# Performance work log

Measured on AMD Instinct MI355X. Metric: run time of the kernel, lower is better.

## Reference

```python
import jax, jax.numpy as jnp
import numpy as np

HIDDEN = 1024
HEADS = 16
HEAD = HIDDEN // HEADS


def setup_inputs() -> dict:
    key = jax.random.key(0)
    k1, k2, k3, k4, k5, k6 = jax.random.split(key, 6)
    B, S = 2, 2048
    x = jax.random.normal(k1, (B, S, HIDDEN), dtype=jnp.float32)
    mask = jax.random.randint(k2, (B, S), 0, 2, dtype=jnp.int32)
    # torch nn.Linear params: W [out,in], b [out]
    s = 1.0 / np.sqrt(HIDDEN)
    qkv_w = jax.random.uniform(k3, (3 * HIDDEN, HIDDEN), jnp.float32, -s, s)
    qkv_b = jax.random.uniform(k4, (3 * HIDDEN,), jnp.float32, -s, s)
    out_w = jax.random.uniform(k5, (HIDDEN, HIDDEN), jnp.float32, -s, s)
    out_b = jax.random.uniform(k6, (HIDDEN,), jnp.float32, -s, s)
    return {"x": x, "mask": mask, "qkv_w": qkv_w, "qkv_b": qkv_b,
            "out_w": out_w, "out_b": out_b}


def reference(x, mask, qkv_w, qkv_b, out_w, out_b):
    B, S, H = x.shape
    scale = HEAD ** -0.5
    qkv = x @ qkv_w.T + qkv_b                      # [B,S,3H]
    qkv = qkv.reshape(B, S, 3, HEADS, HEAD)
    qkv = jnp.transpose(qkv, (2, 0, 3, 1, 4))      # [3,B,h,S,d]
    q, k, v = qkv[0], qkv[1], qkv[2]
    scores = jnp.einsum('bhqd,bhkd->bhqk', q, k) * scale
    # key-padding mask [B,S] -> [B,1,1,S]
    scores = jnp.where(mask[:, None, None, :] == 0, -1e9, scores)
    attn = jax.nn.softmax(scores, axis=-1)
    # dropout is identity in eval mode
    ctx = jnp.einsum('bhqk,bhkd->bhqd', attn, v)   # [B,h,S,d]
    ctx = jnp.transpose(ctx, (0, 2, 1, 3)).reshape(B, S, H)
    return ctx @ out_w.T + out_b
```

## Files before the change

### kernel.cpp

```cpp
#include <hip/hip_runtime.h>
#include <hip/hip_bf16.h>

#define S_LEN 2048
#define NH    16
#define HD    64
#define HID   1024
#define BATCH 2
#define STK   72

typedef __bf16 bf16x8 __attribute__((ext_vector_type(8)));
typedef float  f32x4  __attribute__((ext_vector_type(4)));

__device__ __forceinline__ unsigned int pk2(float lo, float hi) {
    union { __hip_bfloat162 h; unsigned int u; } c;
    c.h = __float22bfloat162_rn(make_float2(lo, hi));
    return c.u;
}
__device__ __forceinline__ uint4 pk8(float4 a, float4 b) {
    uint4 o;
    o.x = pk2(a.x, a.y); o.y = pk2(a.z, a.w);
    o.z = pk2(b.x, b.y); o.w = pk2(b.z, b.w);
    return o;
}
__device__ __forceinline__ float exp2_hw(float x) {
    float r; asm("v_exp_f32 %0, %1" : "=v"(r) : "v"(x)); return r;
}
__device__ __forceinline__ void gll16(const unsigned short* g, unsigned short* l) {
    __builtin_amdgcn_global_load_lds(
        (const __attribute__((address_space(1))) void*)g,
        (__attribute__((address_space(3))) void*)l, 16, 0, 0);
}

__global__ __launch_bounds__(256)
void fill_constf(float* __restrict__ out, long n, float v) {
    long i = (long)blockIdx.x * 256 + threadIdx.x;
    const long stride = (long)gridDim.x * 256;
    for (; i < n; i += stride) out[i] = v;
}

__global__ __launch_bounds__(256)
void cvt_bf16(const float* __restrict__ src, unsigned short* __restrict__ dst, long n8) {
    long t = (long)blockIdx.x * 256 + threadIdx.x;
    const long stride = (long)gridDim.x * 256;
    for (; t < n8; t += stride) {
        const float4 a = *(const float4*)(src + t * 8);
        const float4 b = *(const float4*)(src + t * 8 + 4);
        *(uint4*)(dst + t * 8) = pk8(a, b);
    }
}
__global__ __launch_bounds__(256)
void cvt2_bf16(const float* __restrict__ s0, unsigned short* __restrict__ d0, long n0,
               const float* __restrict__ s1, unsigned short* __restrict__ d1, long n1) {
    long t = (long)blockIdx.x * 256 + threadIdx.x;
    const long stride = (long)gridDim.x * 256;
    for (; t < n0 + n1; t += stride) {
        const float* s; unsigned short* d; long i;
        if (t < n0) { s = s0; d = d0; i = t; } else { s = s1; d = d1; i = t - n0; }
        const float4 a = *(const float4*)(s + i * 8);
        const float4 b = *(const float4*)(s + i * 8 + 4);
        *(uint4*)(d + i * 8) = pk8(a, b);
    }
}

__global__ __launch_bounds__(256)
void gemm_bf16(const unsigned short* __restrict__ A,
               const unsigned short* __restrict__ W,
               const float* __restrict__ bias,
               unsigned short* __restrict__ o0,
               unsigned short* __restrict__ o1,
               unsigned short* __restrict__ o2,
               float* __restrict__ of,
               int mode)
{
    __shared__ __align__(16) unsigned short lA[128 * 32];
    __shared__ __align__(16) unsigned short lB[128 * 32];
    const int tid  = threadIdx.x;
    const int lane = tid & 63, wv = tid >> 6;
    const int quad = lane >> 4, l16 = lane & 15;
    const int wm = (wv & 1) * 64, wn = (wv >> 1) * 64;
    const int m0 = blockIdx.y * 128, n0 = blockIdx.x * 128;

    f32x4 acc[4][4] = {};

    const int srow0 = wv * 32 + (lane >> 2);
    const int srow1 = srow0 + 16;
    const int sc    = (lane & 3) * 8;
    const unsigned short* pa0 = A + (long)(m0 + srow0) * HID + sc;
    const unsigned short* pa1 = A + (long)(m0 + srow1) * HID + sc;
    const unsigned short* pb0 = W + (long)(n0 + srow0) * HID + sc;
    const unsigned short* pb1 = W + (long)(n0 + srow1) * HID + sc;
    unsigned short* la0 = &lA[(wv * 2 + 0) * 512];
    unsigned short* la1 = &lA[(wv * 2 + 1) * 512];
    unsigned short* lb0 = &lB[(wv * 2 + 0) * 512];
    unsigned short* lb1 = &lB[(wv * 2 + 1) * 512];

    for (int k0 = 0; k0 < HID; k0 += 32) {
        gll16(pa0 + k0, la0);
        gll16(pa1 + k0, la1);
        gll16(pb0 + k0, lb0);
        gll16(pb1 + k0, lb1);
        __syncthreads();

        bf16x8 af[4], bfr[4];
#pragma unroll
        for (int mt = 0; mt < 4; mt++)
            af[mt] = *(const bf16x8*)&lA[(wm + mt * 16 + l16) * 32 + quad * 8];
#pragma unroll
        for (int nt = 0; nt < 4; nt++)
            bfr[nt] = *(const bf16x8*)&lB[(wn + nt * 16 + l16) * 32 + quad * 8];
#pragma unroll
        for (int mt = 0; mt < 4; mt++)
#pragma unroll
            for (int nt = 0; nt < 4; nt++)
                acc[mt][nt] = __builtin_amdgcn_mfma_f32_16x16x32_bf16(
                    af[mt], bfr[nt], acc[mt][nt], 0, 0, 0);
        __syncthreads();
    }

    if (mode == 0) {
#pragma unroll
        for (int nt = 0; nt < 4; nt++) {
            const int n = n0 + wn + nt * 16 + l16;
            const float bv = bias[n];
            const int part = n >> 10, f = n & 1023, h = f >> 6, d = f & 63;
#pragma unroll
            for (int mt = 0; mt < 4; mt++) {
                const int mbase = m0 + wm + mt * 16 + quad * 4;
                const int b = mbase >> 11, s0 = mbase & 2047;
                const int bh = b * NH + h;
                if (part == 2) {
                    uint2 o;
                    o.x = pk2(acc[mt][nt][0] + bv, acc[mt][nt][1] + bv);
                    o.y = pk2(acc[mt][nt][2] + bv, acc[mt][nt][3] + bv);
                    *(uint2*)&o2[((long)bh * HD + d) * S_LEN + s0] = o;
                } else {
                    unsigned short* dst = (part == 0) ? o0 : o1;
#pragma unroll
                    for (int r = 0; r < 4; r++) {
                        union { __hip_bfloat16 h; unsigned short u; } cv;
                        cv.h = __float2bfloat16(acc[mt][nt][r] + bv);
                        dst[((long)bh * S_LEN + s0 + r) * HD + d] = cv.u;
                    }
                }
            }
        }
    } else {
#pragma unroll
        for (int nt = 0; nt < 4; nt++) {
            const int n = n0 + wn + nt * 16 + l16;
            const float bv = bias[n];
#pragma unroll
            for (int mt = 0; mt < 4; mt++) {
                const int mbase = m0 + wm + mt * 16 + quad * 4;
#pragma unroll
                for (int r = 0; r < 4; r++)
                    of[(long)(mbase + r) * HID + n] = acc[mt][nt][r] + bv;
            }
        }
    }
}

__global__ __launch_bounds__(512)
void attn(const unsigned short* __restrict__ q,
          const unsigned short* __restrict__ k,
          const unsigned short* __restrict__ vt_g,
          const int* __restrict__ mask,
          unsigned short* __restrict__ ctx)
{
    __shared__ __align__(16) unsigned short kt[64 * STK];
    __shared__ __align__(16) unsigned short vt[64 * STK];
    __shared__ __align__(16) __bf16 pt[8][16 * 72];
    __shared__ float mkv[64];

    const int tid  = threadIdx.x;
    const int lane = tid & 63, wv = tid >> 6;
    const int quad = lane >> 4, l16 = lane & 15;
    const int qt = blockIdx.x, h = blockIdx.y, b = blockIdx.z;
    const int bh = b * NH + h;
    const float SC = 0.18033688f;

    const int sq = qt * 128 + wv * 16 + l16;
    bf16x8 qf0 = *(const bf16x8*)&q[((long)bh * S_LEN + sq) * HD + quad * 8];
    bf16x8 qf1 = *(const bf16x8*)&q[((long)bh * S_LEN + sq) * HD + 32 + quad * 8];

    float mrun = -1e30f, lrun = 0.f;
    f32x4 Of[4] = {};

    const int sr = tid >> 3, sc8 = (tid & 7) * 8;
    const unsigned short* kg = k    + ((long)bh * S_LEN + sr) * HD + sc8;
    const unsigned short* vg = vt_g + ((long)bh * HD + sr) * S_LEN + sc8;
    __bf16* ptw = pt[wv];

    uint4 rk = *(const uint4*)(kg);
    uint4 rv = *(const uint4*)(vg);
    float rm = 0.f;
    if (tid < 64) rm = (mask[b * S_LEN + tid] == 0) ? -1e9f : 0.f;

    for (int k0 = 0; k0 < S_LEN; k0 += 64) {
        *(uint4*)&kt[sr * STK + sc8] = rk;
        *(uint4*)&vt[sr * STK + sc8] = rv;
        if (tid < 64) mkv[tid] = rm;
        if (k0 + 64 < S_LEN) {
            rk = *(const uint4*)(kg + (long)(k0 + 64) * HD);
            rv = *(const uint4*)(vg + (k0 + 64));
            if (tid < 64) rm = (mask[b * S_LEN + k0 + 64 + tid] == 0) ? -1e9f : 0.f;
        }
        __syncthreads();

        float st[4][4];
#pragma unroll
        for (int nt = 0; nt < 4; nt++) {
            bf16x8 k0f = *(const bf16x8*)&kt[(nt * 16 + l16) * STK + quad * 8];
            bf16x8 k1f = *(const bf16x8*)&kt[(nt * 16 + l16) * STK + 32 + quad * 8];
            f32x4 s = {};
            s = __builtin_amdgcn_mfma_f32_16x16x32_bf16(k0f, qf0, s, 0, 0, 0);
            s = __builtin_amdgcn_mfma_f32_16x16x32_bf16(k1f, qf1, s, 0, 0, 0);
            const float4 mv = *(const float4*)&mkv[nt * 16 + quad * 4];
#pragma unroll
            for (int r = 0; r < 4; r++) st[nt][r] = fmaf(s[r], SC, (&mv.x)[r]);
        }

        float mx = st[0][0];
#pragma unroll
        for (int nt = 0; nt < 4; nt++)
#pragma unroll
            for (int r = 0; r < 4; r++) mx = fmaxf(mx, st[nt][r]);
        mx = fmaxf(mx, __shfl_xor(mx, 16, 64));
        mx = fmaxf(mx, __shfl_xor(mx, 32, 64));
        const float mn = fmaxf(mrun, mx);
        const float alpha = exp2_hw(mrun - mn);
        float pr[4][4];
#pragma unroll
        for (int nt = 0; nt < 4; nt++)
#pragma unroll
            for (int r = 0; r < 4; r++) pr[nt][r] = exp2_hw(st[nt][r] - mn);
        float rs = 0.f;
#pragma unroll
        for (int nt = 0; nt < 4; nt++)
#pragma unroll
            for (int r = 0; r < 4; r++) rs += pr[nt][r];
        rs += __shfl_xor(rs, 16, 64);
        rs += __shfl_xor(rs, 32, 64);
        lrun = lrun * alpha + rs;
        mrun = mn;

#pragma unroll
        for (int nt = 0; nt < 4; nt++) {
            const unsigned long long lo = pk2(pr[nt][0], pr[nt][1]);
            const unsigned long long hi = pk2(pr[nt][2], pr[nt][3]);
            *(unsigned long long*)&ptw[l16 * 72 + nt * 16 + quad * 4] = lo | (hi << 32);
        }
        asm volatile("" ::: "memory");

#pragma unroll
        for (int nt = 0; nt < 4; nt++) Of[nt] *= alpha;

#pragma unroll
        for (int ks = 0; ks < 2; ks++) {
            bf16x8 bp = *(const bf16x8*)&ptw[l16 * 72 + ks * 32 + quad * 8];
#pragma unroll
            for (int nt = 0; nt < 4; nt++) {
                bf16x8 av = *(const bf16x8*)&vt[(nt * 16 + l16) * STK + ks * 32 + quad * 8];
                Of[nt] = __builtin_amdgcn_mfma_f32_16x16x32_bf16(av, bp, Of[nt], 0, 0, 0);
            }
        }
        __syncthreads();
    }

    const float inv = 1.f / lrun;
#pragma unroll
    for (int nt = 0; nt < 4; nt++) {
        uint2 o;
        o.x = pk2(Of[nt][0] * inv, Of[nt][1] * inv);
        o.y = pk2(Of[nt][2] * inv, Of[nt][3] * inv);
        *(uint2*)&ctx[((long)b * S_LEN + sq) * HID + h * HD + nt * 16 + quad * 4] = o;
    }
}

extern "C" void kernel_launch(void* const* d_in, const int* in_sizes, int n_in,
                              void* d_out, int out_size, void* d_ws, size_t ws_size,
                              hipStream_t stream) {
    float* outp = (float*)d_out;

    const float* x = nullptr; const int* mask = nullptr;
    const float* qkv_w = nullptr; const float* qkv_b = nullptr;
    const float* out_w = nullptr; const float* out_b = nullptr;
    for (int i = 0; i < n_in; i++) {
        switch (in_sizes[i]) {
            case 4194304: x     = (const float*)d_in[i]; break;
            case 4096:    mask  = (const int*)d_in[i];   break;
            case 3145728: qkv_w = (const float*)d_in[i]; break;
            case 3072:    qkv_b = (const float*)d_in[i]; break;
            case 1048576: out_w = (const float*)d_in[i]; break;
            case 1024:    out_b = (const float*)d_in[i]; break;
            default: break;
        }
    }
    if (!x || !mask || !qkv_w || !qkv_b || !out_w || !out_b) {
        fill_constf<<<256, 256, 0, stream>>>(outp, (long)out_size, 1000.0f);
        return;
    }

    const size_t per = (size_t)BATCH * NH * S_LEN * HD;
    const size_t nx  = (size_t)BATCH * S_LEN * HID;
    const size_t nqw = (size_t)3 * HID * HID;
    const size_t now = (size_t)HID * HID;
    if (ws_size < 4 * per * sizeof(unsigned short)) {
        fill_constf<<<256, 256, 0, stream>>>(outp, (long)out_size, 2000.0f);
        return;
    }

    unsigned short* wsq = (unsigned short*)d_ws;
    unsigned short* wsk = wsq + per;
    unsigned short* wsv = wsk + per;
    unsigned short* wsc = wsv + per;
    unsigned short* xb  = wsc;
    unsigned short* qwb = (unsigned short*)d_out;
    unsigned short* owb = wsq;

    cvt2_bf16<<<1024, 256, 0, stream>>>(x, xb, (long)(nx / 8), qkv_w, qwb, (long)(nqw / 8));
    gemm_bf16<<<dim3(3 * HID / 128, BATCH * S_LEN / 128), 256, 0, stream>>>(
        xb, qwb, qkv_b, wsq, wsk, wsv, nullptr, 0);
    attn<<<dim3(S_LEN / 128, NH, BATCH), 512, 0, stream>>>(wsq, wsk, wsv, mask, wsc);
    cvt_bf16<<<512, 256, 0, stream>>>(out_w, owb, (long)(now / 8));
    gemm_bf16<<<dim3(HID / 128, BATCH * S_LEN / 128), 256, 0, stream>>>(
        wsc, owb, out_b, nullptr, nullptr, nullptr, outp, 1);
}
```

Measured before the change: 235.7 us.

## Triple-buffer GEMM LDS loads with swizzled layout and XCD-aware block remap

Rewrites the bf16 GEMM main loop to use three LDS buffers with global-to-LDS loads issued two k-steps ahead. Each step waits on vmcnt instead of a full syncthreads pair, so load latency can overlap the MFMA work. It also XOR-swizzles LDS columns to cut bank conflicts and remaps block IDs so neighbouring tiles land on the same XCD for better L2 reuse. In exchange, LDS use per block triples, which may lower occupancy, and the single barrier per iteration relies on the three-buffer rotation to avoid overwriting data another wave is still reading.

```diff
diff --git a/kernel.cpp b/kernel.cpp
--- a/kernel.cpp
+++ b/kernel.cpp
@@ -72,50 +72,72 @@
                float* __restrict__ of,
                int mode)
 {
-    __shared__ __align__(16) unsigned short lA[128 * 32];
-    __shared__ __align__(16) unsigned short lB[128 * 32];
+    __shared__ __align__(16) unsigned short lA[3][128 * 32];
+    __shared__ __align__(16) unsigned short lB[3][128 * 32];
     const int tid  = threadIdx.x;
     const int lane = tid & 63, wv = tid >> 6;
     const int quad = lane >> 4, l16 = lane & 15;
     const int wm = (wv & 1) * 64, wn = (wv >> 1) * 64;
-    const int m0 = blockIdx.y * 128, n0 = blockIdx.x * 128;
+
+    const int nwg = gridDim.x * gridDim.y;
+    const int bid = blockIdx.y * gridDim.x + blockIdx.x;
+    const int xcd = bid & 7, boff = bid >> 3;
+    const int qd = nwg >> 3, rm = nwg & 7;
+    const int swz = (xcd < rm ? xcd * (qd + 1) : rm * (qd + 1) + (xcd - rm) * qd) + boff;
+    const int m0 = (swz / gridDim.x) * 128, n0 = (swz % gridDim.x) * 128;
 
     f32x4 acc[4][4] = {};
 
     const int srow0 = wv * 32 + (lane >> 2);
     const int srow1 = srow0 + 16;
-    const int sc    = (lane & 3) * 8;
-    const unsigned short* pa0 = A + (long)(m0 + srow0) * HID + sc;
-    const unsigned short* pa1 = A + (long)(m0 + srow1) * HID + sc;
-    const unsigned short* pb0 = W + (long)(n0 + srow0) * HID + sc;
-    const unsigned short* pb1 = W + (long)(n0 + srow1) * HID + sc;
-    unsigned short* la0 = &lA[(wv * 2 + 0) * 512];
-    unsigned short* la1 = &lA[(wv * 2 + 1) * 512];
-    unsigned short* lb0 = &lB[(wv * 2 + 0) * 512];
-    unsigned short* lb1 = &lB[(wv * 2 + 1) * 512];
-
+    const int csrc  = ((lane & 3) ^ ((lane >> 3) & 3)) * 8;
+    const unsigned short* pa0 = A + (long)(m0 + srow0) * HID + csrc;
+    const unsigned short* pa1 = A + (long)(m0 + srow1) * HID + csrc;
+    const unsigned short* pb0 = W + (long)(n0 + srow0) * HID + csrc;
+    const unsigned short* pb1 = W + (long)(n0 + srow1) * HID + csrc;
+
+    const int cq8 = (quad ^ ((l16 >> 1) & 3)) * 8;
+
+#define STAGE_G(bufi, koff)                                        \
+    do {                                                           \
+        gll16(pa0 + (koff), &lA[bufi][(wv * 2 + 0) * 512]);        \
+        gll16(pa1 + (koff), &lA[bufi][(wv * 2 + 1) * 512]);        \
+        gll16(pb0 + (koff), &lB[bufi][(wv * 2 + 0) * 512]);        \
+        gll16(pb1 + (koff), &lB[bufi][(wv * 2 + 1) * 512]);        \
+    } while (0)
+
+    STAGE_G(0, 0);
+    STAGE_G(1, 32);
+
+    int cur = 0;
     for (int k0 = 0; k0 < HID; k0 += 32) {
-        gll16(pa0 + k0, la0);
-        gll16(pa1 + k0, la1);
-        gll16(pb0 + k0, lb0);
-        gll16(pb1 + k0, lb1);
-        __syncthreads();
+        if (k0 + 32 < HID) { asm volatile("s_waitcnt vmcnt(4)" ::: "memory"); }
+        else               { asm volatile("s_waitcnt vmcnt(0)" ::: "memory"); }
+        __builtin_amdgcn_s_barrier();
+        asm volatile("" ::: "memory");
+
+        if (k0 + 64 < HID) {
+            const int nxt = cur ? cur - 1 : 2;
+            STAGE_G(nxt, k0 + 64);
+        }
 
         bf16x8 af[4], bfr[4];
 #pragma unroll
         for (int mt = 0; mt < 4; mt++)
-            af[mt] = *(const bf16x8*)&lA[(wm + mt * 16 + l16) * 32 + quad * 8];
+            af[mt] = *(const bf16x8*)&lA[cur][(wm + mt * 16 + l16) * 32 + cq8];
 #pragma unroll
         for (int nt = 0; nt < 4; nt++)
-            bfr[nt] = *(const bf16x8*)&lB[(wn + nt * 16 + l16) * 32 + quad * 8];
+            bfr[nt] = *(const bf16x8*)&lB[cur][(wn + nt * 16 + l16) * 32 + cq8];
 #pragma unroll
         for (int mt = 0; mt < 4; mt++)
 #pragma unroll
             for (int nt = 0; nt < 4; nt++)
                 acc[mt][nt] = __builtin_amdgcn_mfma_f32_16x16x32_bf16(
                     af[mt], bfr[nt], acc[mt][nt], 0, 0, 0);
-        __syncthreads();
-    }
+
+        cur = (cur < 2) ? cur + 1 : 0;
+    }
+#undef STAGE_G
 
     if (mode == 0) {
 #pragma unroll
```

New measurement: 236.7 us. No clear change (+0.4%).
